# Performance work log

Hardware: AMD Instinct MI355X
Metric: run time of the kernel (lower is better)

Reference implementation:

```python
import jax, jax.numpy as jnp
import numpy as np

N_NODES = 40000
N_EDGES = 640000
IN_CH = 128
OUT_CH = 128
NUM_RBF = 64


def setup_inputs() -> dict:
    key = jax.random.key(0)
    ks = jax.random.split(key, 8)
    x = jax.random.normal(ks[0], (N_NODES, IN_CH), dtype=jnp.float32)
    edge_index = jax.random.randint(ks[1], (2, N_EDGES), 0, N_NODES, dtype=jnp.int64)
    edge_rbf = jax.random.uniform(ks[2], (N_EDGES, NUM_RBF), dtype=jnp.float32)
    s1 = 1.0 / np.sqrt(NUM_RBF)
    s2 = 1.0 / np.sqrt(OUT_CH)
    sl = 1.0 / np.sqrt(IN_CH)
    W1 = jax.random.normal(ks[3], (NUM_RBF, OUT_CH), dtype=jnp.float32) * s1
    b1 = jnp.zeros((OUT_CH,), dtype=jnp.float32)
    W2 = jax.random.normal(ks[4], (OUT_CH, OUT_CH), dtype=jnp.float32) * s2
    b2 = jnp.zeros((OUT_CH,), dtype=jnp.float32)
    Wl = jax.random.normal(ks[5], (IN_CH, OUT_CH), dtype=jnp.float32) * sl
    bl = jnp.zeros((OUT_CH,), dtype=jnp.float32)
    return {"x": x, "edge_index": edge_index, "edge_rbf": edge_rbf,
            "W1": W1, "b1": b1, "W2": W2, "b2": b2, "Wl": Wl, "bl": bl}


def reference(x, edge_index, edge_rbf, W1, b1, W2, b2, Wl, bl):
    # filter_net: Linear -> ReLU -> Linear on edge RBF features  [E, OUT_CH]
    weight = jnp.maximum(edge_rbf @ W1 + b1, 0.0) @ W2 + b2
    # node linear projection  [N, OUT_CH]
    h = x @ Wl + bl
    row, col = edge_index[0], edge_index[1]
    # gather source node features, modulate by continuous filter
    msg = h[col] * weight  # [E, OUT_CH]
    # scatter-sum messages onto destination nodes
    out = jax.ops.segment_sum(msg, row, num_segments=x.shape[0])
    return out
```

## Files before the change

### kernel.cpp

```cpp
#include <hip/hip_runtime.h>
#include <hip/hip_bf16.h>


#define N_NODES 40000
#define N_EDGES 640000
#define IN_CH 128
#define OUT_CH 128
#define NUM_RBF 64

#define TILE_M 64
#define NTILES (N_EDGES / TILE_M)
#define RBF_STR 72
#define T_STR 136
#define HV_STR 136
#define W1_STR 72
#define W2_STR 136
#define NSCB ((N_NODES + 255) / 256)

typedef __attribute__((ext_vector_type(8))) short bf16x8;
typedef __attribute__((ext_vector_type(16))) float f32x16;

__device__ __forceinline__ unsigned short f2bf(float f) {
  unsigned u = __float_as_uint(f);
  return (unsigned short)((u + 0x7FFFu + ((u >> 16) & 1u)) >> 16);
}
__device__ __forceinline__ float bf2f(unsigned short s) {
  return __uint_as_float(((unsigned)s) << 16);
}

__global__ __launch_bounds__(256) void node_linear_mfma(
    const float* __restrict__ x, const float* __restrict__ Wl,
    const float* __restrict__ bl, unsigned short* __restrict__ hbf) {
  __shared__ __align__(16) char pool[IN_CH * W2_STR * 2];
  const int t = threadIdx.x;
  const int lane = t & 63;
  const int l31 = lane & 31;
  const int lhalf = lane >> 5;
  const int wv = t >> 6;

  {
    unsigned short* sWT = (unsigned short*)pool;
    const int k2 = t >> 1;
    const int d0 = (t & 1) * 64;
#pragma unroll
    for (int i = 0; i < 16; ++i) {
      float4 v = *(const float4*)(Wl + k2 * OUT_CH + d0 + 4 * i);
      sWT[(d0 + 4 * i + 0) * W2_STR + k2] = f2bf(v.x);
      sWT[(d0 + 4 * i + 1) * W2_STR + k2] = f2bf(v.y);
      sWT[(d0 + 4 * i + 2) * W2_STR + k2] = f2bf(v.z);
      sWT[(d0 + 4 * i + 3) * W2_STR + k2] = f2bf(v.w);
    }
  }
  __syncthreads();
  const int nbase = wv * 32 + l31;
  bf16x8 BW[8];
  {
    const unsigned short* sWT = (const unsigned short*)pool;
#pragma unroll
    for (int kk = 0; kk < 8; ++kk)
      BW[kk] = *(const bf16x8*)&sWT[nbase * W2_STR + kk * 16 + lhalf * 8];
  }
  const float blv = bl[nbase];
  __syncthreads();

  const int rbase = blockIdx.x * TILE_M;
  unsigned short* sX = (unsigned short*)pool;
  {
    const int m = t >> 2;
    const int c0 = (t & 3) * 32;
    const float* src = x + (size_t)(rbase + m) * IN_CH + c0;
#pragma unroll
    for (int i = 0; i < 8; ++i) {
      float4 v = *(const float4*)(src + 4 * i);
      ushort4 p;
      p.x = f2bf(v.x); p.y = f2bf(v.y); p.z = f2bf(v.z); p.w = f2bf(v.w);
      *(ushort4*)&sX[m * T_STR + c0 + 4 * i] = p;
    }
  }
  __syncthreads();
#pragma unroll
  for (int mt = 0; mt < 2; ++mt) {
    f32x16 acc = {0.f, 0.f, 0.f, 0.f, 0.f, 0.f, 0.f, 0.f,
                  0.f, 0.f, 0.f, 0.f, 0.f, 0.f, 0.f, 0.f};
#pragma unroll
    for (int kk = 0; kk < 8; ++kk) {
      bf16x8 A = *(const bf16x8*)&sX[(mt * 32 + l31) * T_STR + kk * 16 + lhalf * 8];
      acc = __builtin_amdgcn_mfma_f32_32x32x16_bf16(A, BW[kk], acc, 0, 0, 0);
    }
#pragma unroll
    for (int r = 0; r < 16; ++r) {
      const int rowm = mt * 32 + (r & 3) + 8 * (r >> 2) + 4 * lhalf;
      hbf[(size_t)(rbase + rowm) * OUT_CH + nbase] = f2bf(acc[r] + blv);
    }
  }
}

__global__ void hist_kernel(const int* __restrict__ rowI, int* __restrict__ count) {
  int e = blockIdx.x * 256 + threadIdx.x;
  if (e < N_EDGES) atomicAdd(&count[rowI[e]], 1);
}

__global__ __launch_bounds__(256) void scan1_kernel(const int* __restrict__ count,
                                                    int* __restrict__ tscan,
                                                    int* __restrict__ bsum) {
  __shared__ int s[256];
  const int t = threadIdx.x;
  const int i = blockIdx.x * 256 + t;
  const int v = (i < N_NODES) ? count[i] : 0;
  s[t] = v;
  __syncthreads();
  for (int off = 1; off < 256; off <<= 1) {
    int u = (t >= off) ? s[t - off] : 0;
    __syncthreads();
    s[t] += u;
    __syncthreads();
  }
  if (i < N_NODES) tscan[i] = s[t];
  if (t == 255) bsum[blockIdx.x] = s[255];
}

__global__ __launch_bounds__(256) void scan2_kernel(const int* __restrict__ bsum,
                                                    int* __restrict__ boff) {
  __shared__ int s[256];
  const int t = threadIdx.x;
  const int v = (t < NSCB) ? bsum[t] : 0;
  s[t] = v;
  __syncthreads();
  for (int off = 1; off < 256; off <<= 1) {
    int u = (t >= off) ? s[t - off] : 0;
    __syncthreads();
    s[t] += u;
    __syncthreads();
  }
  if (t < NSCB) boff[t] = s[t] - v;
}

__global__ __launch_bounds__(256) void scan3_kernel(
    const int* __restrict__ count, const int* __restrict__ tscan,
    const int* __restrict__ boff, int* __restrict__ cursor,
    int* __restrict__ row_ptr) {
  const int i = blockIdx.x * 256 + threadIdx.x;
  if (i < N_NODES) {
    const int ex = boff[blockIdx.x] + tscan[i] - count[i];
    cursor[i] = ex;
    row_ptr[i] = ex;
  }
  if (i == 0) row_ptr[N_NODES] = N_EDGES;
}

__global__ void scatter_kernel(const int* __restrict__ rowI, int* __restrict__ cursor,
                               int* __restrict__ spos) {
  int e = blockIdx.x * 256 + threadIdx.x;
  if (e < N_EDGES) spos[e] = atomicAdd(&cursor[rowI[e]], 1);
}

template <bool ATOMIC>
__global__ __launch_bounds__(256, 3) void edge_filter_kernel(
    const int* __restrict__ eidx, const float* __restrict__ rbf,
    const float* __restrict__ W1, const float* __restrict__ b1,
    const float* __restrict__ W2, const float* __restrict__ b2,
    const unsigned short* __restrict__ hbf, const int* __restrict__ aux,
    unsigned short* __restrict__ msg, float* __restrict__ outp) {
  __shared__ __align__(16) char pool[IN_CH * W2_STR * 2];
  __shared__ __align__(16) unsigned short sHv[TILE_M * HV_STR];
  __shared__ int sAux[TILE_M];

  unsigned short* sT = (unsigned short*)pool;
  unsigned short* sRbf = (unsigned short*)(pool + TILE_M * T_STR * 2);
  unsigned short* sMsg = (unsigned short*)(pool + TILE_M * T_STR * 2);

  const int t = threadIdx.x;
  const int lane = t & 63;
  const int l31 = lane & 31;
  const int lhalf = lane >> 5;
  const int wv = t >> 6;
  const int nbase = wv * 32 + l31;

  {
    unsigned short* sW1T = (unsigned short*)pool;
    const int k = t >> 2;
    const int c0 = (t & 3) * 32;
#pragma unroll
    for (int i = 0; i < 8; ++i) {
      float4 v = *(const float4*)(W1 + k * OUT_CH + c0 + 4 * i);
      sW1T[(c0 + 4 * i + 0) * W1_STR + k] = f2bf(v.x);
      sW1T[(c0 + 4 * i + 1) * W1_STR + k] = f2bf(v.y);
      sW1T[(c0 + 4 * i + 2) * W1_STR + k] = f2bf(v.z);
      sW1T[(c0 + 4 * i + 3) * W1_STR + k] = f2bf(v.w);
    }
  }
  __syncthreads();
  bf16x8 B1[4];
  {
    const unsigned short* sW1T = (const unsigned short*)pool;
#pragma unroll
    for (int kk = 0; kk < 4; ++kk)
      B1[kk] = *(const bf16x8*)&sW1T[nbase * W1_STR + kk * 16 + lhalf * 8];
  }
  __syncthreads();
  {
    unsigned short* sW2T = (unsigned short*)pool;
    const int k2 = t >> 1;
    const int d0 = (t & 1) * 64;
#pragma unroll
    for (int i = 0; i < 16; ++i) {
      float4 v = *(const float4*)(W2 + k2 * OUT_CH + d0 + 4 * i);
      sW2T[(d0 + 4 * i + 0) * W2_STR + k2] = f2bf(v.x);
      sW2T[(d0 + 4 * i + 1) * W2_STR + k2] = f2bf(v.y);
      sW2T[(d0 + 4 * i + 2) * W2_STR + k2] = f2bf(v.z);
      sW2T[(d0 + 4 * i + 3) * W2_STR + k2] = f2bf(v.w);
    }
  }
  __syncthreads();
  bf16x8 B2[8];
  {
    const unsigned short* sW2T = (const unsigned short*)pool;
#pragma unroll
    for (int kk = 0; kk < 8; ++kk)
      B2[kk] = *(const bf16x8*)&sW2T[nbase * W2_STR + kk * 16 + lhalf * 8];
  }
  const float b1v = b1[nbase];
  const float b2v = b2[nbase];

  const int* colI = eidx + N_EDGES;

  for (int tile = blockIdx.x; tile < NTILES; tile += gridDim.x) {
    const int ebase = tile * TILE_M;
    __syncthreads();

    {
      const int m = t >> 2;
      const int kq = (t & 3) * 16;
      const float* src = rbf + (size_t)(ebase + m) * NUM_RBF + kq;
#pragma unroll
      for (int i = 0; i < 4; ++i) {
        float4 v = *(const float4*)(src + 4 * i);
        ushort4 p;
        p.x = f2bf(v.x); p.y = f2bf(v.y); p.z = f2bf(v.z); p.w = f2bf(v.w);
        *(ushort4*)&sRbf[m * RBF_STR + kq + 4 * i] = p;
      }
#pragma unroll
      for (int i = 0; i < 4; ++i) {
        const int chunk = t + 256 * i;
        const int row = chunk >> 4;
        const int c8 = (chunk & 15) * 8;
        const int col = colI[ebase + row];
        *(uint4*)&sHv[row * HV_STR + c8] =
            *(const uint4*)(hbf + (size_t)col * OUT_CH + c8);
      }
      if (t < TILE_M) sAux[t] = aux[ebase + t];
    }
    __syncthreads();

#pragma unroll
    for (int mt = 0; mt < 2; ++mt) {
      f32x16 acc = {0.f, 0.f, 0.f, 0.f, 0.f, 0.f, 0.f, 0.f,
                    0.f, 0.f, 0.f, 0.f, 0.f, 0.f, 0.f, 0.f};
#pragma unroll
      for (int kk = 0; kk < 4; ++kk) {
        bf16x8 A = *(const bf16x8*)&sRbf[(mt * 32 + l31) * RBF_STR + kk * 16 + lhalf * 8];
        acc = __builtin_amdgcn_mfma_f32_32x32x16_bf16(A, B1[kk], acc, 0, 0, 0);
      }
#pragma unroll
      for (int r = 0; r < 16; ++r) {
        const int rowm = (r & 3) + 8 * (r >> 2) + 4 * lhalf;
        float v = acc[r] + b1v;
        v = v > 0.f ? v : 0.f;
        sT[(mt * 32 + rowm) * T_STR + nbase] = f2bf(v);
      }
    }
    __syncthreads();

    float hv[2][16];
#pragma unroll
    for (int mt = 0; mt < 2; ++mt)
#pragma unroll
      for (int r = 0; r < 16; ++r) {
        const int rowm = mt * 32 + (r & 3) + 8 * (r >> 2) + 4 * lhalf;
        hv[mt][r] = bf2f(sHv[rowm * HV_STR + nbase]);
      }

#pragma unroll
    for (int mt = 0; mt < 2; ++mt) {
      f32x16 acc = {0.f, 0.f, 0.f, 0.f, 0.f, 0.f, 0.f, 0.f,
                    0.f, 0.f, 0.f, 0.f, 0.f, 0.f, 0.f, 0.f};
#pragma unroll
      for (int kk = 0; kk < 8; ++kk) {
        bf16x8 A = *(const bf16x8*)&sT[(mt * 32 + l31) * T_STR + kk * 16 + lhalf * 8];
        acc = __builtin_amdgcn_mfma_f32_32x32x16_bf16(A, B2[kk], acc, 0, 0, 0);
      }
#pragma unroll
      for (int r = 0; r < 16; ++r) {
        const int rowm = mt * 32 + (r & 3) + 8 * (r >> 2) + 4 * lhalf;
        const float m = hv[mt][r] * (acc[r] + b2v);
        if (ATOMIC) {
          atomicAdd(&outp[(size_t)sAux[rowm] * OUT_CH + nbase], m);
        } else {
          sMsg[rowm * T_STR + nbase] = f2bf(m);
        }
      }
    }

    if (!ATOMIC) {
      __syncthreads();
      const int m = t >> 2;
      unsigned short* dst = msg + (size_t)sAux[m] * OUT_CH;
#pragma unroll
      for (int i = 0; i < 4; ++i) {
        const int j = ((t & 3) * 4 + i) * 8;
        *(ushort4*)(dst + j) = *(const ushort4*)&sMsg[m * T_STR + j];
        *(ushort4*)(dst + j + 4) = *(const ushort4*)&sMsg[m * T_STR + j + 4];
      }
    }
  }
}

__global__ __launch_bounds__(256) void segment_reduce_kernel(
    const unsigned short* __restrict__ msg, const int* __restrict__ row_ptr,
    float* __restrict__ out) {
  const int t = threadIdx.x;
  const int wv = t >> 6;
  const int lane = t & 63;
  const int n = blockIdx.x * 4 + wv;
  const int ebeg = row_ptr[n];
  const int eend = row_ptr[n + 1];
  const unsigned* p = (const unsigned*)msg;

  float a0 = 0.f, a1 = 0.f;
  int e = ebeg;
  for (; e + 4 <= eend; e += 4) {
    unsigned v0 = p[(size_t)(e + 0) * 64 + lane];
    unsigned v1 = p[(size_t)(e + 1) * 64 + lane];
    unsigned v2 = p[(size_t)(e + 2) * 64 + lane];
    unsigned v3 = p[(size_t)(e + 3) * 64 + lane];
    a0 += bf2f((unsigned short)(v0 & 0xffff)) + bf2f((unsigned short)(v1 & 0xffff)) +
          bf2f((unsigned short)(v2 & 0xffff)) + bf2f((unsigned short)(v3 & 0xffff));
    a1 += bf2f((unsigned short)(v0 >> 16)) + bf2f((unsigned short)(v1 >> 16)) +
          bf2f((unsigned short)(v2 >> 16)) + bf2f((unsigned short)(v3 >> 16));
  }
  for (; e < eend; ++e) {
    unsigned v = p[(size_t)e * 64 + lane];
    a0 += bf2f((unsigned short)(v & 0xffff));
    a1 += bf2f((unsigned short)(v >> 16));
  }
  float2 r;
  r.x = a0;
  r.y = a1;
  *(float2*)&out[(size_t)n * OUT_CH + lane * 2] = r;
}

extern "C" void kernel_launch(void* const* d_in, const int* in_sizes, int n_in,
                              void* d_out, int out_size, void* d_ws, size_t ws_size,
                              hipStream_t stream) {
  const float* x    = (const float*)d_in[0];
  const int*   eidx = (const int*)d_in[1];
  const float* rbf  = (const float*)d_in[2];
  const float* W1   = (const float*)d_in[3];
  const float* b1   = (const float*)d_in[4];
  const float* W2   = (const float*)d_in[5];
  const float* b2   = (const float*)d_in[6];
  const float* Wl   = (const float*)d_in[7];
  const float* bl   = (const float*)d_in[8];
  float* out = (float*)d_out;

  char* ws = (char*)d_ws;
  const size_t HBF_B = (size_t)N_NODES * OUT_CH * 2;
  const size_t MSG_B = (size_t)N_EDGES * OUT_CH * 2;
  const size_t SPOS_B = (size_t)N_EDGES * 4;
  const size_t CNT_B = (size_t)N_NODES * 4;
  const size_t RP_B = CNT_B + 64;
  const size_t BS_B = 4 * 256;
  const size_t need =
      HBF_B + MSG_B + SPOS_B + CNT_B * 3 + RP_B + 2 * BS_B + 64;

  size_t off = 0;
  unsigned short* hbf = (unsigned short*)(ws + off); off += HBF_B;
  unsigned short* msg = (unsigned short*)(ws + off); off += MSG_B;
  int* spos    = (int*)(ws + off); off += SPOS_B;
  int* count   = (int*)(ws + off); off += CNT_B;
  int* cursor  = (int*)(ws + off); off += CNT_B;
  int* tscan   = (int*)(ws + off); off += CNT_B;
  int* row_ptr = (int*)(ws + off); off += RP_B;
  int* bsum    = (int*)(ws + off); off += BS_B;
  int* boff    = (int*)(ws + off); off += BS_B;

  node_linear_mfma<<<N_NODES / TILE_M, 256, 0, stream>>>(x, Wl, bl, hbf);

  if (ws_size >= need) {
    hipMemsetAsync(count, 0, CNT_B, stream);
    hist_kernel<<<(N_EDGES + 255) / 256, 256, 0, stream>>>(eidx, count);
    scan1_kernel<<<NSCB, 256, 0, stream>>>(count, tscan, bsum);
    scan2_kernel<<<1, 256, 0, stream>>>(bsum, boff);
    scan3_kernel<<<NSCB, 256, 0, stream>>>(count, tscan, boff, cursor, row_ptr);
    scatter_kernel<<<(N_EDGES + 255) / 256, 256, 0, stream>>>(eidx, cursor, spos);
    edge_filter_kernel<false><<<2500, 256, 0, stream>>>(
        eidx, rbf, W1, b1, W2, b2, hbf, spos, msg, nullptr);
    segment_reduce_kernel<<<N_NODES / 4, 256, 0, stream>>>(msg, row_ptr, out);
  } else {
    hipMemsetAsync(out, 0, (size_t)N_NODES * OUT_CH * sizeof(float), stream);
    edge_filter_kernel<true><<<2500, 256, 0, stream>>>(
        eidx, rbf, W1, b1, W2, b2, hbf, eidx , nullptr, out);
  }
}
```

Before: 438.4 us.

## Fuse segment reduction into edge kernel via sorted edges and run-length atomics

Result: faster. 399.4 us (-8.9%).

```diff
diff --git a/kernel.cpp b/kernel.cpp
--- a/kernel.cpp
+++ b/kernel.cpp
@@ -1,5 +1,4 @@
 #include <hip/hip_runtime.h>
-#include <hip/hip_bf16.h>
 
 
 #define N_NODES 40000
@@ -16,6 +15,7 @@
 #define W1_STR 72
 #define W2_STR 136
 #define NSCB ((N_NODES + 255) / 256)
+#define EDGE_GRID 1024
 
 typedef __attribute__((ext_vector_type(8))) short bf16x8;
 typedef __attribute__((ext_vector_type(16))) float f32x16;
@@ -137,37 +137,39 @@
 
 __global__ __launch_bounds__(256) void scan3_kernel(
     const int* __restrict__ count, const int* __restrict__ tscan,
-    const int* __restrict__ boff, int* __restrict__ cursor,
-    int* __restrict__ row_ptr) {
+    const int* __restrict__ boff, int* __restrict__ cursor) {
   const int i = blockIdx.x * 256 + threadIdx.x;
-  if (i < N_NODES) {
-    const int ex = boff[blockIdx.x] + tscan[i] - count[i];
-    cursor[i] = ex;
-    row_ptr[i] = ex;
-  }
-  if (i == 0) row_ptr[N_NODES] = N_EDGES;
-}
-
-__global__ void scatter_kernel(const int* __restrict__ rowI, int* __restrict__ cursor,
-                               int* __restrict__ spos) {
+  if (i < N_NODES) cursor[i] = boff[blockIdx.x] + tscan[i] - count[i];
+}
+
+__global__ void scatter_kernel(const int* __restrict__ rowI,
+                               const int* __restrict__ colI,
+                               int* __restrict__ cursor,
+                               int* __restrict__ eperm, int* __restrict__ dsts,
+                               int* __restrict__ cols) {
   int e = blockIdx.x * 256 + threadIdx.x;
-  if (e < N_EDGES) spos[e] = atomicAdd(&cursor[rowI[e]], 1);
-}
-
-template <bool ATOMIC>
-__global__ __launch_bounds__(256, 3) void edge_filter_kernel(
-    const int* __restrict__ eidx, const float* __restrict__ rbf,
+  if (e < N_EDGES) {
+    const int r = rowI[e];
+    const int p = atomicAdd(&cursor[r], 1);
+    eperm[p] = e;
+    dsts[p] = r;
+    cols[p] = colI[e];
+  }
+}
+
+template <bool SORTED>
+__global__ __launch_bounds__(256, 4) void edge_fused_kernel(
+    const int* __restrict__ eperm, const float* __restrict__ rbf,
     const float* __restrict__ W1, const float* __restrict__ b1,
     const float* __restrict__ W2, const float* __restrict__ b2,
-    const unsigned short* __restrict__ hbf, const int* __restrict__ aux,
-    unsigned short* __restrict__ msg, float* __restrict__ outp) {
+    const unsigned short* __restrict__ hbf, const int* __restrict__ dsts,
+    const int* __restrict__ cols, float* __restrict__ outp) {
   __shared__ __align__(16) char pool[IN_CH * W2_STR * 2];
-  __shared__ __align__(16) unsigned short sHv[TILE_M * HV_STR];
-  __shared__ int sAux[TILE_M];
-
+
+  unsigned short* sHv = (unsigned short*)pool;
   unsigned short* sT = (unsigned short*)pool;
-  unsigned short* sRbf = (unsigned short*)(pool + TILE_M * T_STR * 2);
-  unsigned short* sMsg = (unsigned short*)(pool + TILE_M * T_STR * 2);
+  unsigned short* sRbf = (unsigned short*)(pool + TILE_M * HV_STR * 2);
+  int* sAux = (int*)(pool + TILE_M * HV_STR * 2 + TILE_M * RBF_STR * 2);
 
   const int t = threadIdx.x;
   const int lane = t & 63;
@@ -222,16 +224,15 @@
   const float b1v = b1[nbase];
   const float b2v = b2[nbase];
 
-  const int* colI = eidx + N_EDGES;
-
   for (int tile = blockIdx.x; tile < NTILES; tile += gridDim.x) {
     const int ebase = tile * TILE_M;
     __syncthreads();
 
     {
       const int m = t >> 2;
+      const int ep = SORTED ? eperm[ebase + m] : (ebase + m);
       const int kq = (t & 3) * 16;
-      const float* src = rbf + (size_t)(ebase + m) * NUM_RBF + kq;
+      const float* src = rbf + (size_t)ep * NUM_RBF + kq;
 #pragma unroll
       for (int i = 0; i < 4; ++i) {
         float4 v = *(const float4*)(src + 4 * i);
@@ -244,12 +245,22 @@
         const int chunk = t + 256 * i;
         const int row = chunk >> 4;
         const int c8 = (chunk & 15) * 8;
-        const int col = colI[ebase + row];
+        const int col = cols[ebase + row];
         *(uint4*)&sHv[row * HV_STR + c8] =
             *(const uint4*)(hbf + (size_t)col * OUT_CH + c8);
       }
-      if (t < TILE_M) sAux[t] = aux[ebase + t];
-    }
+      if (t < TILE_M) sAux[t] = dsts[ebase + t];
+    }
+    __syncthreads();
+
+    float hv[2][16];
+#pragma unroll
+    for (int mt = 0; mt < 2; ++mt)
+#pragma unroll
+      for (int r = 0; r < 16; ++r) {
+        const int rowm = mt * 32 + (r & 3) + 8 * (r >> 2) + 4 * lhalf;
+        hv[mt][r] = bf2f(sHv[rowm * HV_STR + nbase]);
+      }
     __syncthreads();
 
 #pragma unroll
@@ -271,15 +282,8 @@
     }
     __syncthreads();
 
-    float hv[2][16];
-#pragma unroll
-    for (int mt = 0; mt < 2; ++mt)
-#pragma unroll
-      for (int r = 0; r < 16; ++r) {
-        const int rowm = mt * 32 + (r & 3) + 8 * (r >> 2) + 4 * lhalf;
-        hv[mt][r] = bf2f(sHv[rowm * HV_STR + nbase]);
-      }
-
+    float sum = 0.f;
+    int curd = -1;
 #pragma unroll
     for (int mt = 0; mt < 2; ++mt) {
       f32x16 acc = {0.f, 0.f, 0.f, 0.f, 0.f, 0.f, 0.f, 0.f,
@@ -293,60 +297,18 @@
       for (int r = 0; r < 16; ++r) {
         const int rowm = mt * 32 + (r & 3) + 8 * (r >> 2) + 4 * lhalf;
         const float m = hv[mt][r] * (acc[r] + b2v);
-        if (ATOMIC) {
-          atomicAdd(&outp[(size_t)sAux[rowm] * OUT_CH + nbase], m);
+        const int d = sAux[rowm];
+        if (d != curd) {
+          if (curd >= 0) atomicAdd(&outp[(size_t)curd * OUT_CH + nbase], sum);
+          curd = d;
+          sum = m;
         } else {
-          sMsg[rowm * T_STR + nbase] = f2bf(m);
+          sum += m;
         }
       }
     }
-
-    if (!ATOMIC) {
-      __syncthreads();
-      const int m = t >> 2;
-      unsigned short* dst = msg + (size_t)sAux[m] * OUT_CH;
-#pragma unroll
-      for (int i = 0; i < 4; ++i) {
-        const int j = ((t & 3) * 4 + i) * 8;
-        *(ushort4*)(dst + j) = *(const ushort4*)&sMsg[m * T_STR + j];
-        *(ushort4*)(dst + j + 4) = *(const ushort4*)&sMsg[m * T_STR + j + 4];
-      }
-    }
-  }
-}
-
-__global__ __launch_bounds__(256) void segment_reduce_kernel(
-    const unsigned short* __restrict__ msg, const int* __restrict__ row_ptr,
-    float* __restrict__ out) {
-  const int t = threadIdx.x;
-  const int wv = t >> 6;
-  const int lane = t & 63;
-  const int n = blockIdx.x * 4 + wv;
-  const int ebeg = row_ptr[n];
-  const int eend = row_ptr[n + 1];
-  const unsigned* p = (const unsigned*)msg;
-
-  float a0 = 0.f, a1 = 0.f;
-  int e = ebeg;
-  for (; e + 4 <= eend; e += 4) {
-    unsigned v0 = p[(size_t)(e + 0) * 64 + lane];
-    unsigned v1 = p[(size_t)(e + 1) * 64 + lane];
-    unsigned v2 = p[(size_t)(e + 2) * 64 + lane];
-    unsigned v3 = p[(size_t)(e + 3) * 64 + lane];
-    a0 += bf2f((unsigned short)(v0 & 0xffff)) + bf2f((unsigned short)(v1 & 0xffff)) +
-          bf2f((unsigned short)(v2 & 0xffff)) + bf2f((unsigned short)(v3 & 0xffff));
-    a1 += bf2f((unsigned short)(v0 >> 16)) + bf2f((unsigned short)(v1 >> 16)) +
-          bf2f((unsigned short)(v2 >> 16)) + bf2f((unsigned short)(v3 >> 16));
-  }
-  for (; e < eend; ++e) {
-    unsigned v = p[(size_t)e * 64 + lane];
-    a0 += bf2f((unsigned short)(v & 0xffff));
-    a1 += bf2f((unsigned short)(v >> 16));
-  }
-  float2 r;
-  r.x = a0;
-  r.y = a1;
-  *(float2*)&out[(size_t)n * OUT_CH + lane * 2] = r;
+    atomicAdd(&outp[(size_t)curd * OUT_CH + nbase], sum);
+  }
 }
 
 extern "C" void kernel_launch(void* const* d_in, const int* in_sizes, int n_in,
@@ -365,40 +327,40 @@
 
   char* ws = (char*)d_ws;
   const size_t HBF_B = (size_t)N_NODES * OUT_CH * 2;
-  const size_t MSG_B = (size_t)N_EDGES * OUT_CH * 2;
-  const size_t SPOS_B = (size_t)N_EDGES * 4;
+  const size_t EP_B = (size_t)N_EDGES * 4;
   const size_t CNT_B = (size_t)N_NODES * 4;
-  const size_t RP_B = CNT_B + 64;
   const size_t BS_B = 4 * 256;
-  const size_t need =
-      HBF_B + MSG_B + SPOS_B + CNT_B * 3 + RP_B + 2 * BS_B + 64;
+  const size_t need = HBF_B + 3 * EP_B + 3 * CNT_B + 2 * BS_B + 64;
 
   size_t off = 0;
   unsigned short* hbf = (unsigned short*)(ws + off); off += HBF_B;
-  unsigned short* msg = (unsigned short*)(ws + off); off += MSG_B;
-  int* spos    = (int*)(ws + off); off += SPOS_B;
-  int* count   = (int*)(ws + off); off += CNT_B;
-  int* cursor  = (int*)(ws + off); off += CNT_B;
-  int* tscan   = (int*)(ws + off); off += CNT_B;
-  int* row_ptr = (int*)(ws + off); off += RP_B;
-  int* bsum    = (int*)(ws + off); off += BS_B;
-  int* boff    = (int*)(ws + off); off += BS_B;
-
+  int* eperm  = (int*)(ws + off); off += EP_B;
+  int* dsts   = (int*)(ws + off); off += EP_B;
+  int* cols   = (int*)(ws + off); off += EP_B;
+  int* count  = (int*)(ws + off); off += CNT_B;
+  int* cursor = (int*)(ws + off); off += CNT_B;
+  int* tscan  = (int*)(ws + off); off += CNT_B;
+  int* bsum   = (int*)(ws + off); off += BS_B;
+  int* boff   = (int*)(ws + off); off += BS_B;
+
+  const int* rowI = eidx;
+  const int* colI = eidx + N_EDGES;
+
+  hipMemsetAsync(out, 0, (size_t)N_NODES * OUT_CH * sizeof(float), stream);
   node_linear_mfma<<<N_NODES / TILE_M, 256, 0, stream>>>(x, Wl, bl, hbf);
 
   if (ws_size >= need) {
     hipMemsetAsync(count, 0, CNT_B, stream);
-    hist_kernel<<<(N_EDGES + 255) / 256, 256, 0, stream>>>(eidx, count);
+    hist_kernel<<<(N_EDGES + 255) / 256, 256, 0, stream>>>(rowI, count);
     scan1_kernel<<<NSCB, 256, 0, stream>>>(count, tscan, bsum);
     scan2_kernel<<<1, 256, 0, stream>>>(bsum, boff);
-    scan3_kernel<<<NSCB, 256, 0, stream>>>(count, tscan, boff, cursor, row_ptr);
-    scatter_kernel<<<(N_EDGES + 255) / 256, 256, 0, stream>>>(eidx, cursor, spos);
-    edge_filter_kernel<false><<<2500, 256, 0, stream>>>(
-        eidx, rbf, W1, b1, W2, b2, hbf, spos, msg, nullptr);
-    segment_reduce_kernel<<<N_NODES / 4, 256, 0, stream>>>(msg, row_ptr, out);
+    scan3_kernel<<<NSCB, 256, 0, stream>>>(count, tscan, boff, cursor);
+    scatter_kernel<<<(N_EDGES + 255) / 256, 256, 0, stream>>>(
+        rowI, colI, cursor, eperm, dsts, cols);
+    edge_fused_kernel<true><<<EDGE_GRID, 256, 0, stream>>>(
+        eperm, rbf, W1, b1, W2, b2, hbf, dsts, cols, out);
   } else {
-    hipMemsetAsync(out, 0, (size_t)N_NODES * OUT_CH * sizeof(float), stream);
-    edge_filter_kernel<true><<<2500, 256, 0, stream>>>(
-        eidx, rbf, W1, b1, W2, b2, hbf, eidx , nullptr, out);
-  }
-}
+    edge_fused_kernel<false><<<EDGE_GRID, 256, 0, stream>>>(
+        nullptr, rbf, W1, b1, W2, b2, hbf, rowI, colI, out);
+  }
+}
```
